# Performance work log

Hardware: AMD Instinct MI355X
Metric: run time of the kernel (lower is better)

## Reference

```python
import jax, jax.numpy as jnp
import numpy as np

B, L, H, T, C = 64, 1024, 512, 100, 97


def setup_inputs() -> dict:
    key = jax.random.key(0)
    k1, k2, k3, k4, k5 = jax.random.split(key, 5)
    return {
        "position_fmap": jax.random.normal(k1, (B, L, H), dtype=jnp.float32),
        "origin_fmap": jax.random.normal(k2, (B, L, H), dtype=jnp.float32),
        "pos_emb": jax.random.normal(k3, (T, H), dtype=jnp.float32),
        "W_gen": jax.random.normal(k4, (C, H), dtype=jnp.float32) * (1.0 / np.sqrt(H)),
        "b_gen": jax.random.normal(k5, (C,), dtype=jnp.float32) * 0.01,
    }


def reference(position_fmap, origin_fmap, pos_emb, W_gen, b_gen):
    # The torch loop over t in [0, T) computes, per step, scores = fmap @ emb_t,
    # softmax over L, then context = a^T @ origin_fmap. Batched over all steps:
    scores = jnp.einsum('blh,th->btl', position_fmap, pos_emb)   # [B, T, L]
    attn = jax.nn.softmax(scores, axis=-1)                       # softmax over spatial L
    context = jnp.einsum('btl,blh->bth', attn, origin_fmap)      # [B, T, H]
    # generator: Linear(H -> num_classes)
    return jnp.einsum('bth,ch->btc', context, W_gen) + b_gen     # [B, T, C]
```

## Files before the change

### kernel.cpp

```cpp
#include <hip/hip_runtime.h>
#include <hip/hip_bf16.h>

#define B_   64
#define L_   1024
#define H_   512
#define T_   100
#define C_   97
#define TP_  112

typedef _Float16 h8 __attribute__((ext_vector_type(8)));
typedef __attribute__((ext_vector_type(4))) float f32x4;

__global__ __launch_bounds__(256) void k0_prep(
    const float* __restrict__ emb, const float* __restrict__ W,
    _Float16* __restrict__ embh, _Float16* __restrict__ Wh) {
  const int row = blockIdx.x, tid = threadIdx.x;
  if (row < TP_) {
    for (int j = tid; j < H_; j += 256)
      embh[(size_t)row * H_ + j] =
          (row < T_) ? (_Float16)emb[(size_t)row * H_ + j] : (_Float16)0.f;
  } else {
    const int c = row - TP_;
    for (int j = tid; j < H_; j += 256)
      Wh[(size_t)c * H_ + j] =
          (c < C_) ? (_Float16)W[(size_t)c * H_ + j] : (_Float16)0.f;
  }
}

__global__ __launch_bounds__(256) void k1_scores(
    const float* __restrict__ fmap, const _Float16* __restrict__ embh,
    _Float16* __restrict__ sc, float* __restrict__ part) {
  __shared__ float red_m[4 * TP_];
  __shared__ float red_s[4 * TP_];
  __shared__ float sMb[TP_];
  const int tid = threadIdx.x;
  const int wave = tid >> 6, lane = tid & 63;
  const int quad = lane >> 4, cc = lane & 15;
  const int m0 = blockIdx.x * 128 + wave * 32;

  f32x4 acc0[7], acc1[7];
#pragma unroll
  for (int i = 0; i < 7; ++i) {
    acc0[i] = (f32x4){0.f, 0.f, 0.f, 0.f};
    acc1[i] = (f32x4){0.f, 0.f, 0.f, 0.f};
  }

  const float* a0p = fmap + (size_t)(m0 + cc) * H_ + quad * 8;
  const float* a1p = a0p + (size_t)16 * H_;
#pragma unroll 2
  for (int k = 0; k < H_; k += 32) {
    float4 x0 = *(const float4*)(a0p + k);
    float4 x1 = *(const float4*)(a0p + k + 4);
    float4 y0 = *(const float4*)(a1p + k);
    float4 y1 = *(const float4*)(a1p + k + 4);
    h8 a0, a1;
    a0[0] = (_Float16)x0.x; a0[1] = (_Float16)x0.y;
    a0[2] = (_Float16)x0.z; a0[3] = (_Float16)x0.w;
    a0[4] = (_Float16)x1.x; a0[5] = (_Float16)x1.y;
    a0[6] = (_Float16)x1.z; a0[7] = (_Float16)x1.w;
    a1[0] = (_Float16)y0.x; a1[1] = (_Float16)y0.y;
    a1[2] = (_Float16)y0.z; a1[3] = (_Float16)y0.w;
    a1[4] = (_Float16)y1.x; a1[5] = (_Float16)y1.y;
    a1[6] = (_Float16)y1.z; a1[7] = (_Float16)y1.w;
#pragma unroll
    for (int i = 0; i < 7; ++i) {
      h8 bf = *(const h8*)(embh + (size_t)(i * 16 + cc) * H_ + k + quad * 8);
      acc0[i] = __builtin_amdgcn_mfma_f32_16x16x32_f16(a0, bf, acc0[i], 0, 0, 0);
      acc1[i] = __builtin_amdgcn_mfma_f32_16x16x32_f16(a1, bf, acc1[i], 0, 0, 0);
    }
  }

  float pm[7], ps[7];
#pragma unroll
  for (int i = 0; i < 7; ++i) {
    float m = acc0[i][0];
#pragma unroll
    for (int r = 1; r < 4; ++r) m = fmaxf(m, acc0[i][r]);
#pragma unroll
    for (int r = 0; r < 4; ++r) m = fmaxf(m, acc1[i][r]);
    float s = 0.f;
#pragma unroll
    for (int r = 0; r < 4; ++r) s += __expf(acc0[i][r] - m) + __expf(acc1[i][r] - m);
    pm[i] = m; ps[i] = s;
  }
#pragma unroll
  for (int d = 16; d < 64; d <<= 1) {
#pragma unroll
    for (int i = 0; i < 7; ++i) {
      float om = __shfl_xor(pm[i], d, 64);
      float os = __shfl_xor(ps[i], d, 64);
      float M = fmaxf(pm[i], om);
      ps[i] = ps[i] * __expf(pm[i] - M) + os * __expf(om - M);
      pm[i] = M;
    }
  }
  if (lane < 16) {
#pragma unroll
    for (int i = 0; i < 7; ++i) {
      red_m[wave * TP_ + i * 16 + lane] = pm[i];
      red_s[wave * TP_ + i * 16 + lane] = ps[i];
    }
  }
  __syncthreads();
  if (tid < TP_) {
    float M = red_m[tid], S = red_s[tid];
#pragma unroll
    for (int w = 1; w < 4; ++w) {
      float om = red_m[w * TP_ + tid], os = red_s[w * TP_ + tid];
      float nM = fmaxf(M, om);
      S = S * __expf(M - nM) + os * __expf(om - nM);
      M = nM;
    }
    float* p = part + ((size_t)blockIdx.x * TP_ + tid) * 2;
    p[0] = M; p[1] = S;
    sMb[tid] = M;
  }
  __syncthreads();
#pragma unroll
  for (int i = 0; i < 7; ++i) {
    float mb = sMb[i * 16 + cc];
#pragma unroll
    for (int r = 0; r < 4; ++r) {
      const int row0 = m0 + quad * 4 + r;
      sc[(size_t)row0 * TP_ + i * 16 + cc]        = (_Float16)(acc0[i][r] - mb);
      sc[(size_t)(row0 + 16) * TP_ + i * 16 + cc] = (_Float16)(acc1[i][r] - mb);
    }
  }
}

__global__ __launch_bounds__(256) void k2_softmax(
    const _Float16* __restrict__ sc, const float* __restrict__ part,
    _Float16* __restrict__ attn) {
  __shared__ float sAdj[TP_], sInv[TP_];
  const int b = blockIdx.x >> 3, lblk = blockIdx.x & 7;
  const int tid = threadIdx.x;
  if (tid < TP_) {
    float M = -1e30f, S = 0.f;
    for (int k = 0; k < 8; ++k) {
      const float* p = part + ((size_t)(b * 8 + k) * TP_ + tid) * 2;
      float om = p[0], os = p[1];
      float nM = fmaxf(M, om);
      S = S * __expf(M - nM) + os * __expf(om - nM);
      M = nM;
    }
    sInv[tid] = 1.f / S;
    sAdj[tid] = part[((size_t)(b * 8 + lblk) * TP_ + tid) * 2] - M;
  }
  __syncthreads();
  const _Float16* sp = sc + (size_t)blockIdx.x * (128 * TP_);
  _Float16* ap = attn + (size_t)blockIdx.x * (128 * TP_);
  for (int f = tid * 8; f < 128 * TP_; f += 2048) {
    h8 v = *(const h8*)(sp + f);
    const int t0 = f % TP_;
    h8 o;
#pragma unroll
    for (int j = 0; j < 8; ++j)
      o[j] = (_Float16)(__expf((float)v[j] + sAdj[t0 + j]) * sInv[t0 + j]);
    *(h8*)(ap + f) = o;
  }
}

__global__ __launch_bounds__(256) void k3_context(
    const _Float16* __restrict__ attn, const float* __restrict__ origin,
    float* __restrict__ ctxT) {
  const int b = blockIdx.x >> 3, hb = (blockIdx.x & 7) * 64;
  const int tid = threadIdx.x;
  const int wave = tid >> 6, lane = tid & 63;
  const int quad = lane >> 4, cc = lane & 15;
  const int hA = hb + wave * 16 + cc;

  f32x4 acc[7];
#pragma unroll
  for (int i = 0; i < 7; ++i) acc[i] = (f32x4){0.f, 0.f, 0.f, 0.f};

  const float* op = origin + (size_t)b * L_ * H_ + (size_t)(quad * 8) * H_ + hA;
  const _Float16* bp = attn + (size_t)b * L_ * TP_ + (size_t)(quad * 8) * TP_;

#pragma unroll 2
  for (int l0 = 0; l0 < L_; l0 += 32) {
    h8 a;
#pragma unroll
    for (int j = 0; j < 8; ++j) a[j] = (_Float16)op[(size_t)(l0 + j) * H_];
#pragma unroll
    for (int i = 0; i < 7; ++i) {
      h8 bf;
#pragma unroll
      for (int j = 0; j < 8; ++j) bf[j] = bp[(size_t)(l0 + j) * TP_ + i * 16 + cc];
      acc[i] = __builtin_amdgcn_mfma_f32_16x16x32_f16(a, bf, acc[i], 0, 0, 0);
    }
  }
  const int hrow = hb + wave * 16 + quad * 4;
#pragma unroll
  for (int i = 0; i < 7; ++i)
#pragma unroll
    for (int r = 0; r < 4; ++r)
      ctxT[((size_t)b * H_ + hrow + r) * TP_ + i * 16 + cc] = acc[i][r];
}

__global__ __launch_bounds__(256) void k4_out(
    const float* __restrict__ ctxT, const _Float16* __restrict__ Wh,
    const float* __restrict__ bias, float* __restrict__ out) {
  const int b = blockIdx.x / 7, mt = blockIdx.x % 7;
  const int tid = threadIdx.x;
  const int wave = tid >> 6, lane = tid & 63;
  const int quad = lane >> 4, cc = lane & 15;
  f32x4 acc0 = (f32x4){0.f, 0.f, 0.f, 0.f};
  f32x4 acc1 = (f32x4){0.f, 0.f, 0.f, 0.f};
  const int c0 = wave * 16 + cc;
  const int c1 = (wave + 4) * 16 + cc;
  const bool hasB = (wave < 3);
  const float* apc = ctxT + ((size_t)b * H_ + quad * 8) * TP_ + mt * 16 + cc;
  const _Float16* b0p = Wh + (size_t)c0 * H_ + quad * 8;
  const _Float16* b1p = Wh + (size_t)(hasB ? c1 : c0) * H_ + quad * 8;
  for (int k = 0; k < H_; k += 32) {
    h8 a;
#pragma unroll
    for (int j = 0; j < 8; ++j) a[j] = (_Float16)apc[(size_t)(k + j) * TP_];
    h8 bf0 = *(const h8*)(b0p + k);
    acc0 = __builtin_amdgcn_mfma_f32_16x16x32_f16(a, bf0, acc0, 0, 0, 0);
    if (hasB) {
      h8 bf1 = *(const h8*)(b1p + k);
      acc1 = __builtin_amdgcn_mfma_f32_16x16x32_f16(a, bf1, acc1, 0, 0, 0);
    }
  }
  const float bias0 = (c0 < C_) ? bias[c0] : 0.f;
  const float bias1 = (hasB && c1 < C_) ? bias[c1] : 0.f;
#pragma unroll
  for (int r = 0; r < 4; ++r) {
    const int t = mt * 16 + quad * 4 + r;
    if (t < T_) {
      if (c0 < C_) out[((size_t)b * T_ + t) * C_ + c0] = acc0[r] + bias0;
      if (hasB && c1 < C_) out[((size_t)b * T_ + t) * C_ + c1] = acc1[r] + bias1;
    }
  }
}

extern "C" void kernel_launch(void* const* d_in, const int* in_sizes, int n_in,
                              void* d_out, int out_size, void* d_ws, size_t ws_size,
                              hipStream_t stream) {
  const float* fmap   = (const float*)d_in[0];
  const float* origin = (const float*)d_in[1];
  const float* emb    = (const float*)d_in[2];
  const float* W      = (const float*)d_in[3];
  const float* bias   = (const float*)d_in[4];
  float* out = (float*)d_out;

  char* ws = (char*)d_ws;
  _Float16* embh = (_Float16*)(ws);
  _Float16* Wh   = (_Float16*)(ws + 114688);
  _Float16* sc   = (_Float16*)(ws + 229376);
  float*    part = (float*)   (ws + 14909440);
  _Float16* attn = (_Float16*)(ws + 15368192);
  float*    ctxT = (float*)   (ws + 30048256);

  hipLaunchKernelGGL(k0_prep,    dim3(224), dim3(256), 0, stream, emb, W, embh, Wh);
  hipLaunchKernelGGL(k1_scores,  dim3(512), dim3(256), 0, stream, fmap, embh, sc, part);
  hipLaunchKernelGGL(k2_softmax, dim3(512), dim3(256), 0, stream, sc, part, attn);
  hipLaunchKernelGGL(k3_context, dim3(512), dim3(256), 0, stream, attn, origin, ctxT);
  hipLaunchKernelGGL(k4_out,     dim3(448), dim3(256), 0, stream, ctxT, Wh, bias, out);
}
```

Before: 363.3 us.

## Reassociate generator matmul before context and fuse softmax into final GEMM

```diff
diff --git a/kernel.cpp b/kernel.cpp
--- a/kernel.cpp
+++ b/kernel.cpp
@@ -1,5 +1,4 @@
 #include <hip/hip_runtime.h>
-#include <hip/hip_bf16.h>
 
 #define B_   64
 #define L_   1024
@@ -36,51 +35,36 @@
   const int tid = threadIdx.x;
   const int wave = tid >> 6, lane = tid & 63;
   const int quad = lane >> 4, cc = lane & 15;
-  const int m0 = blockIdx.x * 128 + wave * 32;
-
-  f32x4 acc0[7], acc1[7];
-#pragma unroll
-  for (int i = 0; i < 7; ++i) {
-    acc0[i] = (f32x4){0.f, 0.f, 0.f, 0.f};
-    acc1[i] = (f32x4){0.f, 0.f, 0.f, 0.f};
-  }
-
-  const float* a0p = fmap + (size_t)(m0 + cc) * H_ + quad * 8;
-  const float* a1p = a0p + (size_t)16 * H_;
+  const int m0 = blockIdx.x * 64 + wave * 16;
+
+  f32x4 acc[7];
+#pragma unroll
+  for (int i = 0; i < 7; ++i) acc[i] = (f32x4){0.f, 0.f, 0.f, 0.f};
+
+  const float* ap = fmap + (size_t)(m0 + cc) * H_ + quad * 8;
 #pragma unroll 2
   for (int k = 0; k < H_; k += 32) {
-    float4 x0 = *(const float4*)(a0p + k);
-    float4 x1 = *(const float4*)(a0p + k + 4);
-    float4 y0 = *(const float4*)(a1p + k);
-    float4 y1 = *(const float4*)(a1p + k + 4);
-    h8 a0, a1;
-    a0[0] = (_Float16)x0.x; a0[1] = (_Float16)x0.y;
-    a0[2] = (_Float16)x0.z; a0[3] = (_Float16)x0.w;
-    a0[4] = (_Float16)x1.x; a0[5] = (_Float16)x1.y;
-    a0[6] = (_Float16)x1.z; a0[7] = (_Float16)x1.w;
-    a1[0] = (_Float16)y0.x; a1[1] = (_Float16)y0.y;
-    a1[2] = (_Float16)y0.z; a1[3] = (_Float16)y0.w;
-    a1[4] = (_Float16)y1.x; a1[5] = (_Float16)y1.y;
-    a1[6] = (_Float16)y1.z; a1[7] = (_Float16)y1.w;
+    float4 x0 = *(const float4*)(ap + k);
+    float4 x1 = *(const float4*)(ap + k + 4);
+    h8 a;
+    a[0] = (_Float16)x0.x; a[1] = (_Float16)x0.y;
+    a[2] = (_Float16)x0.z; a[3] = (_Float16)x0.w;
+    a[4] = (_Float16)x1.x; a[5] = (_Float16)x1.y;
+    a[6] = (_Float16)x1.z; a[7] = (_Float16)x1.w;
 #pragma unroll
     for (int i = 0; i < 7; ++i) {
       h8 bf = *(const h8*)(embh + (size_t)(i * 16 + cc) * H_ + k + quad * 8);
-      acc0[i] = __builtin_amdgcn_mfma_f32_16x16x32_f16(a0, bf, acc0[i], 0, 0, 0);
-      acc1[i] = __builtin_amdgcn_mfma_f32_16x16x32_f16(a1, bf, acc1[i], 0, 0, 0);
+      acc[i] = __builtin_amdgcn_mfma_f32_16x16x32_f16(a, bf, acc[i], 0, 0, 0);
     }
   }
 
   float pm[7], ps[7];
 #pragma unroll
   for (int i = 0; i < 7; ++i) {
-    float m = acc0[i][0];
-#pragma unroll
-    for (int r = 1; r < 4; ++r) m = fmaxf(m, acc0[i][r]);
-#pragma unroll
-    for (int r = 0; r < 4; ++r) m = fmaxf(m, acc1[i][r]);
+    float m = fmaxf(fmaxf(acc[i][0], acc[i][1]), fmaxf(acc[i][2], acc[i][3]));
     float s = 0.f;
 #pragma unroll
-    for (int r = 0; r < 4; ++r) s += __expf(acc0[i][r] - m) + __expf(acc1[i][r] - m);
+    for (int r = 0; r < 4; ++r) s += __expf(acc[i][r] - m);
     pm[i] = m; ps[i] = s;
   }
 #pragma unroll
@@ -120,117 +104,132 @@
   for (int i = 0; i < 7; ++i) {
     float mb = sMb[i * 16 + cc];
 #pragma unroll
-    for (int r = 0; r < 4; ++r) {
-      const int row0 = m0 + quad * 4 + r;
-      sc[(size_t)row0 * TP_ + i * 16 + cc]        = (_Float16)(acc0[i][r] - mb);
-      sc[(size_t)(row0 + 16) * TP_ + i * 16 + cc] = (_Float16)(acc1[i][r] - mb);
-    }
-  }
-}
-
-__global__ __launch_bounds__(256) void k2_softmax(
-    const _Float16* __restrict__ sc, const float* __restrict__ part,
-    _Float16* __restrict__ attn) {
-  __shared__ float sAdj[TP_], sInv[TP_];
-  const int b = blockIdx.x >> 3, lblk = blockIdx.x & 7;
+    for (int r = 0; r < 4; ++r)
+      sc[(size_t)(m0 + quad * 4 + r) * TP_ + i * 16 + cc] =
+          (_Float16)(acc[i][r] - mb);
+  }
+}
+
+__global__ __launch_bounds__(256) void k2_gmat(
+    const float* __restrict__ origin, const _Float16* __restrict__ Wh,
+    _Float16* __restrict__ G) {
   const int tid = threadIdx.x;
-  if (tid < TP_) {
+  const int wave = tid >> 6, lane = tid & 63;
+  const int quad = lane >> 4, cc = lane & 15;
+  const int m0 = blockIdx.x * 64 + wave * 16;
+
+  f32x4 acc[7];
+#pragma unroll
+  for (int i = 0; i < 7; ++i) acc[i] = (f32x4){0.f, 0.f, 0.f, 0.f};
+
+  const float* ap = origin + (size_t)(m0 + cc) * H_ + quad * 8;
+#pragma unroll 2
+  for (int k = 0; k < H_; k += 32) {
+    float4 x0 = *(const float4*)(ap + k);
+    float4 x1 = *(const float4*)(ap + k + 4);
+    h8 a;
+    a[0] = (_Float16)x0.x; a[1] = (_Float16)x0.y;
+    a[2] = (_Float16)x0.z; a[3] = (_Float16)x0.w;
+    a[4] = (_Float16)x1.x; a[5] = (_Float16)x1.y;
+    a[6] = (_Float16)x1.z; a[7] = (_Float16)x1.w;
+#pragma unroll
+    for (int i = 0; i < 7; ++i) {
+      h8 bf = *(const h8*)(Wh + (size_t)(i * 16 + cc) * H_ + k + quad * 8);
+      acc[i] = __builtin_amdgcn_mfma_f32_16x16x32_f16(a, bf, acc[i], 0, 0, 0);
+    }
+  }
+#pragma unroll
+  for (int i = 0; i < 7; ++i)
+#pragma unroll
+    for (int r = 0; r < 4; ++r)
+      G[(size_t)(m0 + quad * 4 + r) * TP_ + i * 16 + cc] =
+          (_Float16)acc[i][r];
+}
+
+__global__ __launch_bounds__(512) void k3_fused(
+    const _Float16* __restrict__ sc, const _Float16* __restrict__ G,
+    const float* __restrict__ part, const float* __restrict__ bias,
+    float* __restrict__ out) {
+  __shared__ float sAdj[16][16];
+  __shared__ float sInv[16];
+  __shared__ f32x4 sred[8][4][64];
+  const int bid = blockIdx.x;
+  const int b = bid / 14;
+  const int rem = bid % 14;
+  const int mt = rem >> 1;
+  const int ng = rem & 1;
+  const int NT = ng ? 3 : 4;
+  const int ncol0 = ng * 64;
+  const int tid = threadIdx.x;
+  const int w = tid >> 6, lane = tid & 63;
+  const int quad = lane >> 4, cc = lane & 15;
+
+  if (tid < 16) {
+    const int t = mt * 16 + tid;
+    float mM[16];
     float M = -1e30f, S = 0.f;
-    for (int k = 0; k < 8; ++k) {
-      const float* p = part + ((size_t)(b * 8 + k) * TP_ + tid) * 2;
+#pragma unroll
+    for (int s = 0; s < 16; ++s) {
+      const float* p = part + ((size_t)(b * 16 + s) * TP_ + t) * 2;
       float om = p[0], os = p[1];
+      mM[s] = om;
       float nM = fmaxf(M, om);
       S = S * __expf(M - nM) + os * __expf(om - nM);
       M = nM;
     }
     sInv[tid] = 1.f / S;
-    sAdj[tid] = part[((size_t)(b * 8 + lblk) * TP_ + tid) * 2] - M;
-  }
-  __syncthreads();
-  const _Float16* sp = sc + (size_t)blockIdx.x * (128 * TP_);
-  _Float16* ap = attn + (size_t)blockIdx.x * (128 * TP_);
-  for (int f = tid * 8; f < 128 * TP_; f += 2048) {
-    h8 v = *(const h8*)(sp + f);
-    const int t0 = f % TP_;
-    h8 o;
-#pragma unroll
-    for (int j = 0; j < 8; ++j)
-      o[j] = (_Float16)(__expf((float)v[j] + sAdj[t0 + j]) * sInv[t0 + j]);
-    *(h8*)(ap + f) = o;
-  }
-}
-
-__global__ __launch_bounds__(256) void k3_context(
-    const _Float16* __restrict__ attn, const float* __restrict__ origin,
-    float* __restrict__ ctxT) {
-  const int b = blockIdx.x >> 3, hb = (blockIdx.x & 7) * 64;
-  const int tid = threadIdx.x;
-  const int wave = tid >> 6, lane = tid & 63;
-  const int quad = lane >> 4, cc = lane & 15;
-  const int hA = hb + wave * 16 + cc;
-
-  f32x4 acc[7];
-#pragma unroll
-  for (int i = 0; i < 7; ++i) acc[i] = (f32x4){0.f, 0.f, 0.f, 0.f};
-
-  const float* op = origin + (size_t)b * L_ * H_ + (size_t)(quad * 8) * H_ + hA;
-  const _Float16* bp = attn + (size_t)b * L_ * TP_ + (size_t)(quad * 8) * TP_;
-
+#pragma unroll
+    for (int s = 0; s < 16; ++s) sAdj[s][tid] = mM[s] - M;
+  }
+  __syncthreads();
+
+  f32x4 acc[4];
+#pragma unroll
+  for (int i = 0; i < 4; ++i) acc[i] = (f32x4){0.f, 0.f, 0.f, 0.f};
+
+  const float inv = sInv[cc];
+  const _Float16* scp = sc + (size_t)b * L_ * TP_ + mt * 16 + cc;
+  const _Float16* gp  = G  + (size_t)b * L_ * TP_ + ncol0 + cc;
+  const int kbase = w * 128;
 #pragma unroll 2
-  for (int l0 = 0; l0 < L_; l0 += 32) {
+  for (int l0 = kbase; l0 < kbase + 128; l0 += 32) {
+    const int r0 = l0 + quad * 8;
+    const float adj = sAdj[r0 >> 6][cc];
     h8 a;
 #pragma unroll
-    for (int j = 0; j < 8; ++j) a[j] = (_Float16)op[(size_t)(l0 + j) * H_];
-#pragma unroll
-    for (int i = 0; i < 7; ++i) {
-      h8 bf;
-#pragma unroll
-      for (int j = 0; j < 8; ++j) bf[j] = bp[(size_t)(l0 + j) * TP_ + i * 16 + cc];
-      acc[i] = __builtin_amdgcn_mfma_f32_16x16x32_f16(a, bf, acc[i], 0, 0, 0);
-    }
-  }
-  const int hrow = hb + wave * 16 + quad * 4;
-#pragma unroll
-  for (int i = 0; i < 7; ++i)
-#pragma unroll
-    for (int r = 0; r < 4; ++r)
-      ctxT[((size_t)b * H_ + hrow + r) * TP_ + i * 16 + cc] = acc[i][r];
-}
-
-__global__ __launch_bounds__(256) void k4_out(
-    const float* __restrict__ ctxT, const _Float16* __restrict__ Wh,
-    const float* __restrict__ bias, float* __restrict__ out) {
-  const int b = blockIdx.x / 7, mt = blockIdx.x % 7;
-  const int tid = threadIdx.x;
-  const int wave = tid >> 6, lane = tid & 63;
-  const int quad = lane >> 4, cc = lane & 15;
-  f32x4 acc0 = (f32x4){0.f, 0.f, 0.f, 0.f};
-  f32x4 acc1 = (f32x4){0.f, 0.f, 0.f, 0.f};
-  const int c0 = wave * 16 + cc;
-  const int c1 = (wave + 4) * 16 + cc;
-  const bool hasB = (wave < 3);
-  const float* apc = ctxT + ((size_t)b * H_ + quad * 8) * TP_ + mt * 16 + cc;
-  const _Float16* b0p = Wh + (size_t)c0 * H_ + quad * 8;
-  const _Float16* b1p = Wh + (size_t)(hasB ? c1 : c0) * H_ + quad * 8;
-  for (int k = 0; k < H_; k += 32) {
-    h8 a;
-#pragma unroll
-    for (int j = 0; j < 8; ++j) a[j] = (_Float16)apc[(size_t)(k + j) * TP_];
-    h8 bf0 = *(const h8*)(b0p + k);
-    acc0 = __builtin_amdgcn_mfma_f32_16x16x32_f16(a, bf0, acc0, 0, 0, 0);
-    if (hasB) {
-      h8 bf1 = *(const h8*)(b1p + k);
-      acc1 = __builtin_amdgcn_mfma_f32_16x16x32_f16(a, bf1, acc1, 0, 0, 0);
-    }
-  }
-  const float bias0 = (c0 < C_) ? bias[c0] : 0.f;
-  const float bias1 = (hasB && c1 < C_) ? bias[c1] : 0.f;
-#pragma unroll
-  for (int r = 0; r < 4; ++r) {
-    const int t = mt * 16 + quad * 4 + r;
-    if (t < T_) {
-      if (c0 < C_) out[((size_t)b * T_ + t) * C_ + c0] = acc0[r] + bias0;
-      if (hasB && c1 < C_) out[((size_t)b * T_ + t) * C_ + c1] = acc1[r] + bias1;
+    for (int j = 0; j < 8; ++j) {
+      float sv = (float)scp[(size_t)(r0 + j) * TP_];
+      a[j] = (_Float16)(__expf(sv + adj) * inv);
+    }
+#pragma unroll
+    for (int nt = 0; nt < 4; ++nt) {
+      if (nt < NT) {
+        h8 bf;
+#pragma unroll
+        for (int j = 0; j < 8; ++j)
+          bf[j] = gp[(size_t)(r0 + j) * TP_ + nt * 16];
+        acc[nt] = __builtin_amdgcn_mfma_f32_16x16x32_f16(a, bf, acc[nt], 0, 0, 0);
+      }
+    }
+  }
+
+#pragma unroll
+  for (int nt = 0; nt < 4; ++nt)
+    if (nt < NT) sred[w][nt][lane] = acc[nt];
+  __syncthreads();
+
+  if (w < NT) {
+    f32x4 s = sred[0][w][lane];
+#pragma unroll
+    for (int ww = 1; ww < 8; ++ww) s += sred[ww][w][lane];
+    const int c = ncol0 + w * 16 + cc;
+    if (c < C_) {
+      const float bv = bias[c];
+#pragma unroll
+      for (int r = 0; r < 4; ++r) {
+        const int t = mt * 16 + quad * 4 + r;
+        if (t < T_) out[((size_t)b * T_ + t) * C_ + c] = s[r] + bv;
+      }
     }
   }
 }
@@ -250,12 +249,10 @@
   _Float16* Wh   = (_Float16*)(ws + 114688);
   _Float16* sc   = (_Float16*)(ws + 229376);
   float*    part = (float*)   (ws + 14909440);
-  _Float16* attn = (_Float16*)(ws + 15368192);
-  float*    ctxT = (float*)   (ws + 30048256);
-
-  hipLaunchKernelGGL(k0_prep,    dim3(224), dim3(256), 0, stream, emb, W, embh, Wh);
-  hipLaunchKernelGGL(k1_scores,  dim3(512), dim3(256), 0, stream, fmap, embh, sc, part);
-  hipLaunchKernelGGL(k2_softmax, dim3(512), dim3(256), 0, stream, sc, part, attn);
-  hipLaunchKernelGGL(k3_context, dim3(512), dim3(256), 0, stream, attn, origin, ctxT);
-  hipLaunchKernelGGL(k4_out,     dim3(448), dim3(256), 0, stream, ctxT, Wh, bias, out);
-}
+  _Float16* G    = (_Float16*)(ws + 15826944);
+
+  hipLaunchKernelGGL(k0_prep,   dim3(224),  dim3(256), 0, stream, emb, W, embh, Wh);
+  hipLaunchKernelGGL(k1_scores, dim3(1024), dim3(256), 0, stream, fmap, embh, sc, part);
+  hipLaunchKernelGGL(k2_gmat,   dim3(1024), dim3(256), 0, stream, origin, Wh, G);
+  hipLaunchKernelGGL(k3_fused,  dim3(896),  dim3(512), 0, stream, sc, G, part, bias, out);
+}
```

After: 381.9 us. +5.1%, slower.
